# Optimization experiments

Measured on AMD Instinct MI355X. Metric: run time of the kernel, lower is better.

Reference implementation:

```python
import jax, jax.numpy as jnp
import numpy as np

B, L, D, K, O, DM = 32, 512, 32, 6, 192, 512
Q = 0.75
EPS = 1e-6
BN_EPS = 1e-5


def _torch_median(a, axis):
    # torch.median returns the LOWER of the two middle values for even n
    n = a.shape[axis]
    s = jnp.sort(a, axis=axis)
    return jnp.take(s, jnp.array([(n - 1) // 2]), axis=axis)


def setup_inputs() -> dict:
    key = jax.random.key(0)
    ks = jax.random.split(key, 5)
    return {
        "x": jax.random.normal(ks[0], (B, L, D), jnp.float32),
        "x_date": jax.random.normal(ks[1], (B, L, D, K), jnp.float32),
        "y_date": jax.random.normal(ks[2], (B, O, D, K), jnp.float32),
        "mlp_w1": jax.random.normal(ks[3], (L, DM), jnp.float32) * 0.02,
        "mlp_b1": jnp.zeros((DM,), jnp.float32),
        "mlp_w2": jax.random.normal(ks[4], (DM, 2), jnp.float32) * 0.02,
        "mlp_b2": jnp.zeros((2,), jnp.float32),
        "bn_gamma": jnp.ones((D,), jnp.float32),
        "bn_beta": jnp.zeros((D,), jnp.float32),
    }


def reference(x, x_date, y_date, mlp_w1, mlp_b1, mlp_w2, mlp_b2, bn_gamma, bn_beta):
    k = x_date.shape[-1]
    # robust location/scale (median + interquantile range), reduced over time dim 1
    med_true = _torch_median(x, 1)                 # (B,1,D)
    med_map = _torch_median(x_date, 1)             # (B,1,D,K)
    std_true = (jnp.quantile(x, Q, axis=1, keepdims=True)
                - jnp.quantile(x, 1.0 - Q, axis=1, keepdims=True) + EPS)   # (B,1,D)
    std_map = (jnp.quantile(x_date, Q, axis=1, keepdims=True)
               - jnp.quantile(x_date, 1.0 - Q, axis=1, keepdims=True) + EPS)  # (B,1,D,K)
    x_date_map = (x_date - med_map) / std_map * std_true[..., None] + med_true[..., None]
    y_date_map = (y_date - med_map) / std_map * std_true[..., None] + med_true[..., None]

    # cross-attention over time with tiny contraction dim k
    scores = jnp.einsum('bldk,bodk->bdlo', x_date_map, y_date_map)  # (B,D,L,O)
    A = jax.nn.softmax(scores / jnp.sqrt(jnp.float32(k)), axis=-2)  # softmax over L
    V = jnp.einsum('bld,bdlo->bdo', x, A)                           # (B,D,O)

    # BatchNorm1d(d_feature) in training mode: batch stats over (B, O); dropout = identity (eval)
    mu = jnp.mean(V, axis=(0, 2), keepdims=True)
    var = jnp.var(V, axis=(0, 2), keepdims=True)
    y = (V - mu) * jax.lax.rsqrt(var + BN_EPS) * bn_gamma[None, :, None] + bn_beta[None, :, None]
    y = jnp.transpose(y, (0, 2, 1))                                 # (B,O,D)

    # softmax-gated fusion MLP over the time axis
    error = x - x_date_map.mean(-1)                                 # (B,L,D)
    h = jax.nn.gelu(jnp.einsum('bld,lm->bdm', error, mlp_w1) + mlp_b1, approximate=False)
    w = jax.nn.softmax(h @ mlp_w2 + mlp_b2, axis=-1)                # (B,D,2)

    y_map = jnp.stack([y_date_map.mean(-1), y], axis=-1)            # (B,O,D,2)
    pred = jnp.sum(y_map * w[:, None], axis=-1)                     # (B,O,D)
    return pred
```

## Files before the change

kernel.cpp:

```cpp
#include <hip/hip_runtime.h>
#include <math.h>

#define BB 32
#define LL 512
#define DD 32
#define KK 6
#define OO 192
#define DM 512

typedef __fp16 h2 __attribute__((ext_vector_type(2)));
typedef __fp16 h8 __attribute__((ext_vector_type(8)));
union F2H { float f; h2 h; };
__device__ __forceinline__ float asF(h2 h) { F2H u; u.h = h; return u.f; }
__device__ __forceinline__ h2 asH(float f) { F2H u; u.f = f; return u.h; }

typedef short bf16x8 __attribute__((ext_vector_type(8)));
typedef float f4 __attribute__((ext_vector_type(4)));
union U16x8 { uint4 u; bf16x8 h; };
union UH8F { uint4 u; h8 h; };

__device__ __forceinline__ unsigned short f2bf(float x) {
  unsigned int u = __float_as_uint(x);
  u = (u + 0x7FFF + ((u >> 16) & 1)) >> 16;
  return (unsigned short)u;
}

#define MOVDPP(x, ctrl) \
  __int_as_float(__builtin_amdgcn_mov_dpp(__float_as_int(x), ctrl, 0xf, 0xf, true))

#define CSTR2 524
#define XD0   0
#define XV0   6288
#define MEDO  7336
#define STDO  7350
#define SAO   7364
#define SCO   7376
#define BNR   7388
#define XMP   0
#define YMP   4096
#define LDSF  7404

__device__ __forceinline__ void sort512(float v[8], int lane) {
  #pragma unroll
  for (int k = 2; k <= 512; k <<= 1) {
    #pragma unroll
    for (int j = k >> 1; j > 0; j >>= 1) {
      if (j >= 8) {
        int jj = j >> 3;
        bool lower = (lane & jj) == 0;
        bool asc = ((lane << 3) & k) == 0;
        bool keepmin = (asc == lower);
        #pragma unroll
        for (int r = 0; r < 8; ++r) {
          float o;
          if (jj == 1)      o = MOVDPP(v[r], 0xB1);
          else if (jj == 2) o = MOVDPP(v[r], 0x4E);
          else if (jj == 8) o = MOVDPP(v[r], 0x128);
          else              o = __shfl_xor(v[r], jj);
          v[r] = keepmin ? fminf(v[r], o) : fmaxf(v[r], o);
        }
      } else {
        #pragma unroll
        for (int r = 0; r < 8; ++r) {
          if ((r & j) == 0) {
            int r2 = r | j;
            bool asc = (((lane << 3) | r) & k) == 0;
            float a = v[r], b = v[r2];
            float lo = fminf(a, b), hi = fmaxf(a, b);
            v[r]  = asc ? lo : hi;
            v[r2] = asc ? hi : lo;
          }
        }
      }
    }
  }
}

__global__ __launch_bounds__(256) void fused_kernel(
    const float* __restrict__ x, const float* __restrict__ x_date,
    const float* __restrict__ y_date, const float* __restrict__ w1,
    float* __restrict__ V, float* __restrict__ ymean,
    float* __restrict__ bnp, unsigned short* __restrict__ errb,
    unsigned short* __restrict__ w1t) {
  __shared__ float lds[LDSF];
  int orig = blockIdx.x;
  int tid = threadIdx.x, lane = tid & 63, wv = tid >> 6;

  if (orig >= 512) {
    float* tw = lds;
    int id = orig - 512;
    int l0 = (id & 7) * 64, m0 = (id >> 3) * 64;
    #pragma unroll
    for (int it = 0; it < 4; ++it) {
      int f = tid + it * 256;
      int row = f >> 4, c4 = f & 15;
      float4 v = ((const float4*)(w1 + (size_t)(l0 + row) * DM + m0))[c4];
      float* p = &tw[row * 68 + c4 * 4];
      p[0] = v.x; p[1] = v.y; p[2] = v.z; p[3] = v.w;
    }
    __syncthreads();
    unsigned int* w1t32 = (unsigned int*)w1t;
    #pragma unroll
    for (int it = 0; it < 8; ++it) {
      int f = tid + it * 256;
      int mr = f >> 5, c = f & 31;
      float a = tw[(c * 2 + 0) * 68 + mr];
      float b = tw[(c * 2 + 1) * 68 + mr];
      unsigned int u = (unsigned int)f2bf(a) | ((unsigned int)f2bf(b) << 16);
      w1t32[(size_t)(m0 + mr) * (DM / 2) + (l0 >> 1) + c] = u;
    }
    return;
  }

  int xcd = orig & 7, idx = orig >> 3;
  int b = (xcd << 2) | (idx >> 4);
  int d0 = (idx & 15) << 1;

  const float* xs = x_date + (size_t)b * LL * 192 + d0 * 6;
  #pragma unroll
  for (int it = 0; it < 6; ++it) {
    int f = tid + it * 256;
    int row = f / 3, c4 = f % 3;
    float4 v = ((const float4*)(xs + (size_t)row * 192))[c4];
    int col = c4 * 4;
    lds[XD0 + (col + 0) * CSTR2 + row] = v.x;
    lds[XD0 + (col + 1) * CSTR2 + row] = v.y;
    lds[XD0 + (col + 2) * CSTR2 + row] = v.z;
    lds[XD0 + (col + 3) * CSTR2 + row] = v.w;
  }
  #pragma unroll
  for (int it = 0; it < 2; ++it) {
    int row = tid + it * 256;
    float2 v = *(const float2*)(x + (size_t)(b * LL + row) * DD + d0);
    lds[XV0 + row]         = v.x;
    lds[XV0 + CSTR2 + row] = v.y;
  }

  int dl = wv >> 1, half = wv & 1;
  int dme = d0 + dl;
  float2 yr[3][3];
  if (half == 0) {
    #pragma unroll
    for (int j = 0; j < 3; ++j) {
      const float2* yp = (const float2*)(
          y_date + (((size_t)b * OO + (lane + 64 * j)) * DD + dme) * KK);
      yr[j][0] = yp[0]; yr[j][1] = yp[1]; yr[j][2] = yp[2];
    }
  }
  __syncthreads();

  for (int p = 0; p < 4; ++p) {
    int s = p * 4 + wv;
    if (s < 14) {
      const float4* colp = (s < 12)
          ? (const float4*)&lds[XD0 + s * CSTR2 + lane * 8]
          : (const float4*)&lds[XV0 + (s - 12) * CSTR2 + lane * 8];
      float v[8];
      float4 c0 = colp[0], c1 = colp[1];
      v[0]=c0.x; v[1]=c0.y; v[2]=c0.z; v[3]=c0.w;
      v[4]=c1.x; v[5]=c1.y; v[6]=c1.z; v[7]=c1.w;
      sort512(v, lane);
      float e127 = __shfl(v[7], 15);
      float e128 = __shfl(v[0], 16);
      float e255 = __shfl(v[7], 31);
      float e383 = __shfl(v[7], 47);
      float e384 = __shfl(v[0], 48);
      if (lane == 0) {
        float q25 = e127 + 0.75f * (e128 - e127);
        float q75 = e383 + 0.25f * (e384 - e383);
        lds[MEDO + s] = e255;
        lds[STDO + s] = q75 - q25 + 1e-6f;
      }
    }
  }
  __syncthreads();

  if (tid < 12) {
    int dloc = tid / 6;
    float a = lds[STDO + 12 + dloc] / lds[STDO + tid];
    lds[SAO + tid] = a;
    lds[SCO + tid] = lds[MEDO + 12 + dloc] - lds[MEDO + tid] * a;
  }
  __syncthreads();

  const float PSC = 0.58912435f;

  float4 packed[2][2];
  #pragma unroll
  for (int dli = 0; dli < 2; ++dli) {
    int cb = dli * 6;
    float a0 = lds[SAO+cb+0], a1 = lds[SAO+cb+1], a2 = lds[SAO+cb+2];
    float a3 = lds[SAO+cb+3], a4 = lds[SAO+cb+4], a5 = lds[SAO+cb+5];
    float c0 = lds[SCO+cb+0], c1 = lds[SCO+cb+1], c2 = lds[SCO+cb+2];
    float c3 = lds[SCO+cb+3], c4 = lds[SCO+cb+4], c5 = lds[SCO+cb+5];
    #pragma unroll
    for (int it = 0; it < 2; ++it) {
      int l = tid + it * 256;
      float m0 = a0 * lds[XD0 + (cb + 0) * CSTR2 + l] + c0;
      float m1 = a1 * lds[XD0 + (cb + 1) * CSTR2 + l] + c1;
      float m2 = a2 * lds[XD0 + (cb + 2) * CSTR2 + l] + c2;
      float m3 = a3 * lds[XD0 + (cb + 3) * CSTR2 + l] + c3;
      float m4 = a4 * lds[XD0 + (cb + 4) * CSTR2 + l] + c4;
      float m5 = a5 * lds[XD0 + (cb + 5) * CSTR2 + l] + c5;
      float xvv = lds[XV0 + dli * CSTR2 + l];
      errb[(size_t)((b << 5) | (d0 + dli)) * LL + l] =
          f2bf(xvv - (m0 + m1 + m2 + m3 + m4 + m5) * (1.0f / 6.0f));
      packed[it][dli].x = asF(__builtin_amdgcn_cvt_pkrtz(m0 * PSC, m1 * PSC));
      packed[it][dli].y = asF(__builtin_amdgcn_cvt_pkrtz(m2 * PSC, m3 * PSC));
      packed[it][dli].z = asF(__builtin_amdgcn_cvt_pkrtz(m4 * PSC, m5 * PSC));
      packed[it][dli].w = 0.0f;
    }
  }
  __syncthreads();

  #pragma unroll
  for (int it = 0; it < 2; ++it) {
    int l = tid + it * 256;
    *(float4*)&lds[XMP + (0 * 512 + l) * 4] = packed[it][0];
    *(float4*)&lds[XMP + (1 * 512 + l) * 4] = packed[it][1];
  }
  if (half == 0) {
    float askw[6], cskw[6];
    #pragma unroll
    for (int k = 0; k < 6; ++k) {
      askw[k] = lds[SAO + dl * 6 + k];
      cskw[k] = lds[SCO + dl * 6 + k];
    }
    #pragma unroll
    for (int j = 0; j < 3; ++j) {
      int o = lane + 64 * j;
      float q0 = askw[0] * yr[j][0].x + cskw[0];
      float q1 = askw[1] * yr[j][0].y + cskw[1];
      float q2 = askw[2] * yr[j][1].x + cskw[2];
      float q3 = askw[3] * yr[j][1].y + cskw[3];
      float q4 = askw[4] * yr[j][2].x + cskw[4];
      float q5 = askw[5] * yr[j][2].y + cskw[5];
      ymean[(size_t)((b << 5) | dme) * OO + o] =
          (q0 + q1 + q2 + q3 + q4 + q5) * (1.0f / 6.0f);
      float4 yq;
      yq.x = asF(__builtin_amdgcn_cvt_pkrtz(q0, q1));
      yq.y = asF(__builtin_amdgcn_cvt_pkrtz(q2, q3));
      yq.z = asF(__builtin_amdgcn_cvt_pkrtz(q4, q5));
      yq.w = 0.0f;
      *(float4*)&lds[YMP + (dl * 192 + o) * 4] = yq;
    }
  }
  __syncthreads();

  {
    int l15 = lane & 15, kg = lane >> 4;
    uint4 zero4 = make_uint4(0u, 0u, 0u, 0u);

    UH8F bf[6];
    #pragma unroll
    for (int ot = 0; ot < 6; ++ot) {
      int brow = (half * 6 + ot) * 16 + l15;
      uint4 bu = *(const uint4*)&lds[YMP + (dl * 192 + brow) * 4];
      bf[ot].u = (kg == 0) ? bu : zero4;
    }

    float den[6] = {0.f,0.f,0.f,0.f,0.f,0.f};
    float num[6] = {0.f,0.f,0.f,0.f,0.f,0.f};

    for (int lt = 0; lt < 32; ++lt) {
      UH8F af;
      uint4 au = *(const uint4*)&lds[XMP + (dl * 512 + lt * 16 + l15) * 4];
      af.u = (kg == 0) ? au : zero4;
      int rbase = lt * 16 + kg * 4;
      float xv0 = lds[XV0 + dl * CSTR2 + rbase + 0];
      float xv1 = lds[XV0 + dl * CSTR2 + rbase + 1];
      float xv2 = lds[XV0 + dl * CSTR2 + rbase + 2];
      float xv3 = lds[XV0 + dl * CSTR2 + rbase + 3];
      #pragma unroll
      for (int ot = 0; ot < 6; ++ot) {
        f4 c = __builtin_amdgcn_mfma_f32_16x16x32_f16(
            af.h, bf[ot].h, (f4){0.f, 0.f, 0.f, 0.f}, 0, 0, 0);
        float e0 = exp2f(c[0]), e1 = exp2f(c[1]);
        float e2 = exp2f(c[2]), e3 = exp2f(c[3]);
        den[ot] += (e0 + e1) + (e2 + e3);
        num[ot] += (e0 * xv0 + e1 * xv1) + (e2 * xv2 + e3 * xv3);
      }
    }

    #pragma unroll
    for (int ot = 0; ot < 6; ++ot) {
      den[ot] += __shfl_xor(den[ot], 16);
      den[ot] += __shfl_xor(den[ot], 32);
      num[ot] += __shfl_xor(num[ot], 16);
      num[ot] += __shfl_xor(num[ot], 32);
    }

    float s1 = 0.f, s2 = 0.f;
    if (lane < 16) {
      #pragma unroll
      for (int ot = 0; ot < 6; ++ot) {
        float vv = num[ot] / den[ot];
        V[(size_t)((b << 5) | dme) * OO + half * 96 + ot * 16 + lane] = vv;
        s1 += vv; s2 += vv * vv;
      }
    }
    s1 += __shfl_xor(s1, 1); s1 += __shfl_xor(s1, 2);
    s1 += __shfl_xor(s1, 4); s1 += __shfl_xor(s1, 8);
    s2 += __shfl_xor(s2, 1); s2 += __shfl_xor(s2, 2);
    s2 += __shfl_xor(s2, 4); s2 += __shfl_xor(s2, 8);
    if (lane == 0) { lds[BNR + wv] = s1; lds[BNR + 8 + wv] = s2; }
  }
  __syncthreads();

  if (tid == 0) {
    float S0  = lds[BNR + 0] + lds[BNR + 1];
    float S20 = lds[BNR + 8 + 0] + lds[BNR + 8 + 1];
    float S1  = lds[BNR + 2] + lds[BNR + 3];
    float S21 = lds[BNR + 8 + 2] + lds[BNR + 8 + 3];
    bnp[(d0 << 5) | b]                = S0;
    bnp[1024 + ((d0 << 5) | b)]       = S20;
    bnp[((d0 + 1) << 5) | b]          = S1;
    bnp[1024 + (((d0 + 1) << 5) | b)] = S21;
  }
}

__global__ __launch_bounds__(256) void gate_kernel(
    const unsigned short* __restrict__ errb, const unsigned short* __restrict__ w1t,
    const float* __restrict__ b1, const float* __restrict__ w2,
    float* __restrict__ gatep) {
  __shared__ float part[4][32];
  int orig = blockIdx.x;
  int xcd = orig & 7, idx = orig >> 3;
  int b = (xcd << 2) | (idx >> 3);
  int s = idx & 7;
  int tid = threadIdx.x, lane = tid & 63, wv = tid >> 6;
  int m16 = lane & 15, quad = lane >> 4;
  int mw = s * 64 + wv * 16;
  int r0 = b * 32;

  float b1v = b1[mw + m16];
  float2 w2p = ((const float2*)w2)[mw + m16];
  float w2d = w2p.x - w2p.y;

  f4 acc[2];
  acc[0] = (f4){0.f, 0.f, 0.f, 0.f};
  acc[1] = (f4){0.f, 0.f, 0.f, 0.f};

  const unsigned short* ea = errb + (size_t)(r0 + m16) * DM + quad * 8;
  const unsigned short* eb = ea + 16 * DM;
  const unsigned short* wb = w1t + (size_t)(mw + m16) * DM + quad * 8;

  #pragma unroll
  for (int ks = 0; ks < DM; ks += 32) {
    U16x8 ua0, ua1, ub;
    ua0.u = *(const uint4*)(ea + ks);
    ua1.u = *(const uint4*)(eb + ks);
    ub.u  = *(const uint4*)(wb + ks);
    acc[0] = __builtin_amdgcn_mfma_f32_16x16x32_bf16(ua0.h, ub.h, acc[0], 0, 0, 0);
    acc[1] = __builtin_amdgcn_mfma_f32_16x16x32_bf16(ua1.h, ub.h, acc[1], 0, 0, 0);
  }

  float rsum[2][4];
  #pragma unroll
  for (int rt = 0; rt < 2; ++rt) {
    #pragma unroll
    for (int r = 0; r < 4; ++r) {
      float h = acc[rt][r] + b1v;
      float gg = 0.5f * h * (1.0f + erff(h * 0.70710678f));
      rsum[rt][r] = gg * w2d;
    }
  }
  #pragma unroll
  for (int rt = 0; rt < 2; ++rt) {
    #pragma unroll
    for (int r = 0; r < 4; ++r) {
      rsum[rt][r] += __shfl_xor(rsum[rt][r], 1);
      rsum[rt][r] += __shfl_xor(rsum[rt][r], 2);
      rsum[rt][r] += __shfl_xor(rsum[rt][r], 4);
      rsum[rt][r] += __shfl_xor(rsum[rt][r], 8);
    }
  }
  if (m16 == 0) {
    #pragma unroll
    for (int rt = 0; rt < 2; ++rt)
      #pragma unroll
      for (int r = 0; r < 4; ++r)
        part[wv][rt * 16 + quad * 4 + r] = rsum[rt][r];
  }
  __syncthreads();

  if (tid < 32) {
    float p = part[0][tid] + part[1][tid] + part[2][tid] + part[3][tid];
    gatep[(size_t)(((b << 3) | s) << 5) | tid] = p;
  }
}

__global__ __launch_bounds__(256) void tail_kernel(
    const float* __restrict__ gatep, const float* __restrict__ b2,
    const float* __restrict__ V, const float* __restrict__ ymean,
    const float* __restrict__ bnp,
    const float* __restrict__ gamma, const float* __restrict__ beta,
    float* __restrict__ out) {
  __shared__ float vsh[32 * 28], ysh[32 * 28];
  __shared__ float gsh[32], ssh[32], osh[32];
  int g = blockIdx.x, tid = threadIdx.x;
  int xcd = g & 7, idx = g >> 3;
  int b = (xcd << 2) | (idx >> 3);
  int o0 = (idx & 7) * 24;

  if (tid < 192) {
    int dd = tid / 6, c4 = tid % 6;
    size_t goff = (size_t)(b * DD + dd) * OO + o0;
    float4 v = ((const float4*)(V + goff))[c4];
    float4 y = ((const float4*)(ymean + goff))[c4];
    *(float4*)&vsh[dd * 28 + c4 * 4] = v;
    *(float4*)&ysh[dd * 28 + c4 * 4] = y;
  }

  if (tid < 32) {
    float ld = b2[0] - b2[1];
    #pragma unroll
    for (int s = 0; s < 8; ++s)
      ld += gatep[(size_t)(((b << 3) | s) << 5) | tid];
    gsh[tid] = 1.0f / (1.0f + expf(-ld));
    float S = 0.f, S2 = 0.f;
    const float* pd = bnp + (tid << 5);
    #pragma unroll 8
    for (int bb = 0; bb < 32; ++bb) { S += pd[bb]; S2 += pd[1024 + bb]; }
    const float inv = 1.0f / (BB * OO);
    float mu = S * inv;
    float var = S2 * inv - mu * mu;
    float gg = gamma[tid] * rsqrtf(var + 1e-5f);
    ssh[tid] = gg;
    osh[tid] = beta[tid] - mu * gg;
  }
  __syncthreads();

  if (tid < 192) {
    int op = tid >> 3, c4 = tid & 7;
    float4 r;
    #pragma unroll
    for (int j = 0; j < 4; ++j) {
      int dd = c4 * 4 + j;
      float v  = vsh[dd * 28 + op];
      float ym = ysh[dd * 28 + op];
      float gg = gsh[dd];
      float y  = v * ssh[dd] + osh[dd];
      ((float*)&r)[j] = ym * gg + y * (1.0f - gg);
    }
    ((float4*)(out + (size_t)(b * OO + o0 + op) * DD))[c4] = r;
  }
}

extern "C" void kernel_launch(void* const* d_in, const int* in_sizes, int n_in,
                              void* d_out, int out_size, void* d_ws, size_t ws_size,
                              hipStream_t stream) {
  const float* x      = (const float*)d_in[0];
  const float* x_date = (const float*)d_in[1];
  const float* y_date = (const float*)d_in[2];
  const float* w1     = (const float*)d_in[3];
  const float* b1     = (const float*)d_in[4];
  const float* w2     = (const float*)d_in[5];
  const float* b2     = (const float*)d_in[6];
  const float* gamma  = (const float*)d_in[7];
  const float* beta   = (const float*)d_in[8];
  float* out = (float*)d_out;

  float* ws    = (float*)d_ws;
  float* V     = ws;
  float* ymean = ws + 196608;
  float* bnp   = ws + 393216;
  unsigned short* errb = (unsigned short*)(ws + 395264);
  unsigned short* w1t  = (unsigned short*)(ws + 657408);
  float* gatep = ws + 788480;

  fused_kernel<<<576, 256, 0, stream>>>(x, x_date, y_date, w1,
                                        V, ymean, bnp, errb, w1t);
  gate_kernel<<<256, 256, 0, stream>>>(errb, w1t, b1, w2, gatep);
  tail_kernel<<<256, 256, 0, stream>>>(gatep, b2, V, ymean, bnp,
                                       gamma, beta, out);
}
```

Baseline: 142.5 us.

## Double fused kernel block size and split attention over L across waves

Raises the fused kernel to 512 threads per block, so each of the 8 waves handles one (feature, output-half, L-half) slice of the attention loop instead of 4 waves covering all of L. Partial softmax denominators and numerators are written to new LDS regions and combined afterwards, and the BatchNorm partial sums are recomputed from the combined values. The aim is more parallelism inside a block to hide MFMA and exp latency in the main loop. In exchange it costs extra LDS, an additional barrier and reduction step, and a risk of lower occupancy from the larger block.

```diff
diff --git a/kernel.cpp b/kernel.cpp
--- a/kernel.cpp
+++ b/kernel.cpp
@@ -38,7 +38,9 @@
 #define BNR   7388
 #define XMP   0
 #define YMP   4096
-#define LDSF  7404
+#define DEN   7404
+#define NUM   8172
+#define LDSF  8940
 
 __device__ __forceinline__ void sort512(float v[8], int lane) {
   #pragma unroll
@@ -76,7 +78,7 @@
   }
 }
 
-__global__ __launch_bounds__(256) void fused_kernel(
+__global__ __launch_bounds__(512, 4) void fused_kernel(
     const float* __restrict__ x, const float* __restrict__ x_date,
     const float* __restrict__ y_date, const float* __restrict__ w1,
     float* __restrict__ V, float* __restrict__ ymean,
@@ -91,8 +93,8 @@
     int id = orig - 512;
     int l0 = (id & 7) * 64, m0 = (id >> 3) * 64;
     #pragma unroll
-    for (int it = 0; it < 4; ++it) {
-      int f = tid + it * 256;
+    for (int it = 0; it < 2; ++it) {
+      int f = tid + it * 512;
       int row = f >> 4, c4 = f & 15;
       float4 v = ((const float4*)(w1 + (size_t)(l0 + row) * DM + m0))[c4];
       float* p = &tw[row * 68 + c4 * 4];
@@ -101,8 +103,8 @@
     __syncthreads();
     unsigned int* w1t32 = (unsigned int*)w1t;
     #pragma unroll
-    for (int it = 0; it < 8; ++it) {
-      int f = tid + it * 256;
+    for (int it = 0; it < 4; ++it) {
+      int f = tid + it * 512;
       int mr = f >> 5, c = f & 31;
       float a = tw[(c * 2 + 0) * 68 + mr];
       float b = tw[(c * 2 + 1) * 68 + mr];
@@ -118,8 +120,8 @@
 
   const float* xs = x_date + (size_t)b * LL * 192 + d0 * 6;
   #pragma unroll
-  for (int it = 0; it < 6; ++it) {
-    int f = tid + it * 256;
+  for (int it = 0; it < 3; ++it) {
+    int f = tid + it * 512;
     int row = f / 3, c4 = f % 3;
     float4 v = ((const float4*)(xs + (size_t)row * 192))[c4];
     int col = c4 * 4;
@@ -128,18 +130,16 @@
     lds[XD0 + (col + 2) * CSTR2 + row] = v.z;
     lds[XD0 + (col + 3) * CSTR2 + row] = v.w;
   }
-  #pragma unroll
-  for (int it = 0; it < 2; ++it) {
-    int row = tid + it * 256;
+  {
+    int row = tid;
     float2 v = *(const float2*)(x + (size_t)(b * LL + row) * DD + d0);
     lds[XV0 + row]         = v.x;
     lds[XV0 + CSTR2 + row] = v.y;
   }
 
-  int dl = wv >> 1, half = wv & 1;
-  int dme = d0 + dl;
   float2 yr[3][3];
-  if (half == 0) {
+  if ((wv & 3) == 0) {
+    int dme = d0 + (wv >> 2);
     #pragma unroll
     for (int j = 0; j < 3; ++j) {
       const float2* yp = (const float2*)(
@@ -149,8 +149,8 @@
   }
   __syncthreads();
 
-  for (int p = 0; p < 4; ++p) {
-    int s = p * 4 + wv;
+  for (int p = 0; p < 2; ++p) {
+    int s = p * 8 + wv;
     if (s < 14) {
       const float4* colp = (s < 12)
           ? (const float4*)&lds[XD0 + s * CSTR2 + lane * 8]
@@ -185,41 +185,33 @@
 
   const float PSC = 0.58912435f;
 
-  float4 packed[2][2];
-  #pragma unroll
-  for (int dli = 0; dli < 2; ++dli) {
-    int cb = dli * 6;
-    float a0 = lds[SAO+cb+0], a1 = lds[SAO+cb+1], a2 = lds[SAO+cb+2];
-    float a3 = lds[SAO+cb+3], a4 = lds[SAO+cb+4], a5 = lds[SAO+cb+5];
-    float c0 = lds[SCO+cb+0], c1 = lds[SCO+cb+1], c2 = lds[SCO+cb+2];
-    float c3 = lds[SCO+cb+3], c4 = lds[SCO+cb+4], c5 = lds[SCO+cb+5];
-    #pragma unroll
-    for (int it = 0; it < 2; ++it) {
-      int l = tid + it * 256;
-      float m0 = a0 * lds[XD0 + (cb + 0) * CSTR2 + l] + c0;
-      float m1 = a1 * lds[XD0 + (cb + 1) * CSTR2 + l] + c1;
-      float m2 = a2 * lds[XD0 + (cb + 2) * CSTR2 + l] + c2;
-      float m3 = a3 * lds[XD0 + (cb + 3) * CSTR2 + l] + c3;
-      float m4 = a4 * lds[XD0 + (cb + 4) * CSTR2 + l] + c4;
-      float m5 = a5 * lds[XD0 + (cb + 5) * CSTR2 + l] + c5;
+  float4 packed[2];
+  {
+    int l = tid;
+    #pragma unroll
+    for (int dli = 0; dli < 2; ++dli) {
+      int cb = dli * 6;
+      float m0 = lds[SAO+cb+0] * lds[XD0 + (cb + 0) * CSTR2 + l] + lds[SCO+cb+0];
+      float m1 = lds[SAO+cb+1] * lds[XD0 + (cb + 1) * CSTR2 + l] + lds[SCO+cb+1];
+      float m2 = lds[SAO+cb+2] * lds[XD0 + (cb + 2) * CSTR2 + l] + lds[SCO+cb+2];
+      float m3 = lds[SAO+cb+3] * lds[XD0 + (cb + 3) * CSTR2 + l] + lds[SCO+cb+3];
+      float m4 = lds[SAO+cb+4] * lds[XD0 + (cb + 4) * CSTR2 + l] + lds[SCO+cb+4];
+      float m5 = lds[SAO+cb+5] * lds[XD0 + (cb + 5) * CSTR2 + l] + lds[SCO+cb+5];
       float xvv = lds[XV0 + dli * CSTR2 + l];
       errb[(size_t)((b << 5) | (d0 + dli)) * LL + l] =
           f2bf(xvv - (m0 + m1 + m2 + m3 + m4 + m5) * (1.0f / 6.0f));
-      packed[it][dli].x = asF(__builtin_amdgcn_cvt_pkrtz(m0 * PSC, m1 * PSC));
-      packed[it][dli].y = asF(__builtin_amdgcn_cvt_pkrtz(m2 * PSC, m3 * PSC));
-      packed[it][dli].z = asF(__builtin_amdgcn_cvt_pkrtz(m4 * PSC, m5 * PSC));
-      packed[it][dli].w = 0.0f;
-    }
-  }
-  __syncthreads();
-
-  #pragma unroll
-  for (int it = 0; it < 2; ++it) {
-    int l = tid + it * 256;
-    *(float4*)&lds[XMP + (0 * 512 + l) * 4] = packed[it][0];
-    *(float4*)&lds[XMP + (1 * 512 + l) * 4] = packed[it][1];
-  }
-  if (half == 0) {
+      packed[dli].x = asF(__builtin_amdgcn_cvt_pkrtz(m0 * PSC, m1 * PSC));
+      packed[dli].y = asF(__builtin_amdgcn_cvt_pkrtz(m2 * PSC, m3 * PSC));
+      packed[dli].z = asF(__builtin_amdgcn_cvt_pkrtz(m4 * PSC, m5 * PSC));
+      packed[dli].w = 0.0f;
+    }
+  }
+  __syncthreads();
+
+  *(float4*)&lds[XMP + (0 * 512 + tid) * 4] = packed[0];
+  *(float4*)&lds[XMP + (1 * 512 + tid) * 4] = packed[1];
+  if ((wv & 3) == 0) {
+    int dl = wv >> 2, dme = d0 + dl;
     float askw[6], cskw[6];
     #pragma unroll
     for (int k = 0; k < 6; ++k) {
@@ -248,29 +240,31 @@
   __syncthreads();
 
   {
+    int adl = wv >> 2, oh = (wv >> 1) & 1, lh = wv & 1;
     int l15 = lane & 15, kg = lane >> 4;
     uint4 zero4 = make_uint4(0u, 0u, 0u, 0u);
 
     UH8F bf[6];
     #pragma unroll
     for (int ot = 0; ot < 6; ++ot) {
-      int brow = (half * 6 + ot) * 16 + l15;
-      uint4 bu = *(const uint4*)&lds[YMP + (dl * 192 + brow) * 4];
+      int brow = (oh * 6 + ot) * 16 + l15;
+      uint4 bu = *(const uint4*)&lds[YMP + (adl * 192 + brow) * 4];
       bf[ot].u = (kg == 0) ? bu : zero4;
     }
 
     float den[6] = {0.f,0.f,0.f,0.f,0.f,0.f};
     float num[6] = {0.f,0.f,0.f,0.f,0.f,0.f};
 
-    for (int lt = 0; lt < 32; ++lt) {
+    for (int t = 0; t < 16; ++t) {
+      int lt = lh * 16 + t;
       UH8F af;
-      uint4 au = *(const uint4*)&lds[XMP + (dl * 512 + lt * 16 + l15) * 4];
+      uint4 au = *(const uint4*)&lds[XMP + (adl * 512 + lt * 16 + l15) * 4];
       af.u = (kg == 0) ? au : zero4;
       int rbase = lt * 16 + kg * 4;
-      float xv0 = lds[XV0 + dl * CSTR2 + rbase + 0];
-      float xv1 = lds[XV0 + dl * CSTR2 + rbase + 1];
-      float xv2 = lds[XV0 + dl * CSTR2 + rbase + 2];
-      float xv3 = lds[XV0 + dl * CSTR2 + rbase + 3];
+      float xv0 = lds[XV0 + adl * CSTR2 + rbase + 0];
+      float xv1 = lds[XV0 + adl * CSTR2 + rbase + 1];
+      float xv2 = lds[XV0 + adl * CSTR2 + rbase + 2];
+      float xv3 = lds[XV0 + adl * CSTR2 + rbase + 3];
       #pragma unroll
       for (int ot = 0; ot < 6; ++ot) {
         f4 c = __builtin_amdgcn_mfma_f32_16x16x32_f16(
@@ -289,29 +283,39 @@
       num[ot] += __shfl_xor(num[ot], 16);
       num[ot] += __shfl_xor(num[ot], 32);
     }
-
-    float s1 = 0.f, s2 = 0.f;
     if (lane < 16) {
       #pragma unroll
       for (int ot = 0; ot < 6; ++ot) {
-        float vv = num[ot] / den[ot];
-        V[(size_t)((b << 5) | dme) * OO + half * 96 + ot * 16 + lane] = vv;
-        s1 += vv; s2 += vv * vv;
+        lds[DEN + wv * 96 + ot * 16 + lane] = den[ot];
+        lds[NUM + wv * 96 + ot * 16 + lane] = num[ot];
       }
     }
-    s1 += __shfl_xor(s1, 1); s1 += __shfl_xor(s1, 2);
-    s1 += __shfl_xor(s1, 4); s1 += __shfl_xor(s1, 8);
-    s2 += __shfl_xor(s2, 1); s2 += __shfl_xor(s2, 2);
-    s2 += __shfl_xor(s2, 4); s2 += __shfl_xor(s2, 8);
-    if (lane == 0) { lds[BNR + wv] = s1; lds[BNR + 8 + wv] = s2; }
-  }
-  __syncthreads();
-
+  }
+  __syncthreads();
+
+  float s1 = 0.f, s2 = 0.f;
+  if (tid < 384) {
+    int dl2 = tid / 192, o = tid % 192;
+    int oh2 = o / 96, r96 = o % 96;
+    int wv0 = dl2 * 4 + oh2 * 2;
+    float dsum = lds[DEN + wv0 * 96 + r96] + lds[DEN + (wv0 + 1) * 96 + r96];
+    float nsum = lds[NUM + wv0 * 96 + r96] + lds[NUM + (wv0 + 1) * 96 + r96];
+    float vv = nsum / dsum;
+    V[(size_t)((b << 5) | (d0 + dl2)) * OO + o] = vv;
+    s1 = vv; s2 = vv * vv;
+  }
+  #pragma unroll
+  for (int off = 32; off > 0; off >>= 1) {
+    s1 += __shfl_down(s1, off);
+    s2 += __shfl_down(s2, off);
+  }
+  if (lane == 0) { lds[BNR + wv] = s1; lds[BNR + 8 + wv] = s2; }
+  __syncthreads();
   if (tid == 0) {
-    float S0  = lds[BNR + 0] + lds[BNR + 1];
-    float S20 = lds[BNR + 8 + 0] + lds[BNR + 8 + 1];
-    float S1  = lds[BNR + 2] + lds[BNR + 3];
-    float S21 = lds[BNR + 8 + 2] + lds[BNR + 8 + 3];
+    float S0  = lds[BNR + 0] + lds[BNR + 1] + lds[BNR + 2];
+    float S20 = lds[BNR + 8] + lds[BNR + 9] + lds[BNR + 10];
+    float S1  = lds[BNR + 3] + lds[BNR + 4] + lds[BNR + 5];
+    float S21 = lds[BNR + 11] + lds[BNR + 12] + lds[BNR + 13];
     bnp[(d0 << 5) | b]                = S0;
     bnp[1024 + ((d0 << 5) | b)]       = S20;
     bnp[((d0 + 1) << 5) | b]          = S1;
@@ -469,7 +473,7 @@
   unsigned short* w1t  = (unsigned short*)(ws + 657408);
   float* gatep = ws + 788480;
 
-  fused_kernel<<<576, 256, 0, stream>>>(x, x_date, y_date, w1,
+  fused_kernel<<<576, 512, 0, stream>>>(x, x_date, y_date, w1,
                                         V, ymean, bnp, errb, w1t);
   gate_kernel<<<256, 256, 0, stream>>>(errb, w1t, b1, w2, gatep);
   tail_kernel<<<256, 256, 0, stream>>>(gatep, b2, V, ymean, bnp,
```

New measurement: 138.3 us. 1.03x faster.
